# Optimization experiments

Hardware: AMD Instinct MI355X
Metric: run time of the kernel (lower is better)

## Reference

```python
import jax, jax.numpy as jnp
import numpy as np

B, S, D = 8, 1024, 768
H, HD = 12, 64
FF = 3072
EPS = 1e-5


def layernorm(x, w, b):
    mu = jnp.mean(x, axis=-1, keepdims=True)
    var = jnp.mean(jnp.square(x - mu), axis=-1, keepdims=True)
    return (x - mu) / jnp.sqrt(var + EPS) * w + b


def setup_inputs() -> dict:
    key = jax.random.key(0)
    ks = jax.random.split(key, 16)
    s_in = 1.0 / np.sqrt(D)
    s_p = 1.0 / np.sqrt(H * HD)
    s_ff = 1.0 / np.sqrt(FF)
    return {
        "x": jax.random.normal(ks[0], (B, S, D), dtype=jnp.float32),
        "ln1_w": jnp.ones((D,), jnp.float32),
        "ln1_b": jnp.zeros((D,), jnp.float32),
        "Wq": jax.random.uniform(ks[1], (H, D, HD), jnp.float32, -s_in, s_in),
        "bq": jax.random.uniform(ks[2], (H, HD), jnp.float32, -s_in, s_in),
        "Wk": jax.random.uniform(ks[3], (H, D, HD), jnp.float32, -s_in, s_in),
        "bk": jax.random.uniform(ks[4], (H, HD), jnp.float32, -s_in, s_in),
        "Wv": jax.random.uniform(ks[5], (H, D, HD), jnp.float32, -s_in, s_in),
        "bv": jax.random.uniform(ks[6], (H, HD), jnp.float32, -s_in, s_in),
        "Wp": jax.random.uniform(ks[7], (H * HD, D), jnp.float32, -s_p, s_p),
        "bp": jax.random.uniform(ks[8], (D,), jnp.float32, -s_p, s_p),
        "ln2_w": jnp.ones((D,), jnp.float32),
        "ln2_b": jnp.zeros((D,), jnp.float32),
        "W1": jax.random.uniform(ks[9], (D, FF), jnp.float32, -s_in, s_in),
        "b1": jax.random.uniform(ks[10], (FF,), jnp.float32, -s_in, s_in),
        "W2": jax.random.uniform(ks[11], (FF, D), jnp.float32, -s_ff, s_ff),
        "b2": jax.random.uniform(ks[12], (D,), jnp.float32, -s_ff, s_ff),
    }


def reference(x, ln1_w, ln1_b, Wq, bq, Wk, bk, Wv, bv, Wp, bp,
              ln2_w, ln2_b, W1, b1, W2, b2):
    gelu = lambda t: jax.nn.gelu(t, approximate=False)
    # --- multi-head self attention (NOTE: original never applies scale) ---
    y = layernorm(x, ln1_w, ln1_b)                       # [B,S,D]
    q = jnp.einsum('bsd,hde->bhse', y, Wq) + bq[:, None, :][None]
    k = jnp.einsum('bsd,hde->bhse', y, Wk) + bk[:, None, :][None]
    v = jnp.einsum('bsd,hde->bhse', y, Wv) + bv[:, None, :][None]
    attn = jax.nn.softmax(jnp.einsum('bhse,bhte->bhst', q, k), axis=-1)
    out = jnp.einsum('bhst,bhte->bhse', attn, v)         # [B,H,S,HD]
    out = out.transpose(0, 2, 1, 3).reshape(x.shape[0], x.shape[1], -1)  # concat heads
    y = gelu(out @ Wp + bp)                              # projection + GELU
    x = x + y                                            # residual 1
    # --- MLP block ---
    h = layernorm(x, ln2_w, ln2_b)
    h = gelu(h @ W1 + b1)
    h = gelu(h @ W2 + b2)
    return x + h                                         # residual 2
```

## Files before the change

### kernel.cpp

```cpp
#include <hip/hip_runtime.h>
#include <hip/hip_bf16.h>
#include <math.h>

#define BB 8
#define SS 1024
#define DD 768
#define HH 12
#define HDD 64
#define FFF 3072
#define NROW (BB*SS)
#define QKVN (3*DD)

typedef __hip_bfloat16 bf16;
typedef __bf16 bf16x8 __attribute__((ext_vector_type(8)));
typedef float floatx4 __attribute__((ext_vector_type(4)));

__device__ __forceinline__ float gelu_fast(float x) {
    float u = x * fmaf(0.07135481627f, x * x, 1.595769122f);
    float e = __expf(u);
    return x * e * __builtin_amdgcn_rcpf(e + 1.0f);
}

__device__ __forceinline__ unsigned short f2bfbits(float f) {
    bf16 h = __float2bfloat16(f);
    return __builtin_bit_cast(unsigned short, h);
}

__device__ __forceinline__ void gload16(const void* g, void* l) {
    __builtin_amdgcn_global_load_lds(
        (const __attribute__((address_space(1))) unsigned int*)g,
        (__attribute__((address_space(3))) unsigned int*)l, 16, 0, 0);
}

__global__ __launch_bounds__(256) void ln_kernel(const float* __restrict__ x,
                                                 const float* __restrict__ w,
                                                 const float* __restrict__ b,
                                                 bf16* __restrict__ y) {
    int row = blockIdx.x;
    const float* xr = x + (size_t)row * DD;
    bf16* yr = y + (size_t)row * DD;
    int tid = threadIdx.x;
    float v0 = xr[tid], v1 = xr[tid + 256], v2 = xr[tid + 512];
    __shared__ float red[256], red2[256];
    red[tid]  = v0 + v1 + v2;
    red2[tid] = v0*v0 + v1*v1 + v2*v2;
    __syncthreads();
    for (int off = 128; off > 0; off >>= 1) {
        if (tid < off) { red[tid] += red[tid+off]; red2[tid] += red2[tid+off]; }
        __syncthreads();
    }
    float mu  = red[0] * (1.0f / DD);
    float var = red2[0] * (1.0f / DD) - mu * mu;
    float inv = rsqrtf(var + 1e-5f);
    yr[tid]       = __float2bfloat16((v0 - mu) * inv * w[tid]       + b[tid]);
    yr[tid + 256] = __float2bfloat16((v1 - mu) * inv * w[tid + 256] + b[tid + 256]);
    yr[tid + 512] = __float2bfloat16((v2 - mu) * inv * w[tid + 512] + b[tid + 512]);
}

__global__ __launch_bounds__(256) void transpose_cast(
    const float* __restrict__ src, bf16* __restrict__ dst, int K, int N, int hmode)
{
    __shared__ float t[32][33];
    int k0 = blockIdx.x * 32, n0 = blockIdx.y * 32;
    int tx = threadIdx.x & 31, ty4 = threadIdx.x >> 5;
    #pragma unroll
    for (int i = 0; i < 4; i++) {
        int k = k0 + ty4 * 4 + i;
        int n = n0 + tx;
        size_t si = hmode ? ((size_t)(n >> 6) * K * 64 + (size_t)k * 64 + (n & 63))
                          : ((size_t)k * N + n);
        t[ty4 * 4 + i][tx] = src[si];
    }
    __syncthreads();
    #pragma unroll
    for (int i = 0; i < 4; i++) {
        int n = n0 + ty4 * 4 + i;
        int k = k0 + tx;
        dst[(size_t)n * K + k] = __float2bfloat16(t[tx][ty4 * 4 + i]);
    }
}

__global__ void concat_bias(const float* __restrict__ bq, const float* __restrict__ bk,
                            const float* __restrict__ bv, float* __restrict__ dst) {
    int i = blockIdx.x * 256 + threadIdx.x;
    if (i < DD) { dst[i] = bq[i]; dst[DD + i] = bk[i]; dst[2 * DD + i] = bv[i]; }
}

template<int MT, int KH>
__global__ __launch_bounds__(256) void mfma_gemm(
    const bf16* __restrict__ A, const bf16* __restrict__ Bt,
    const float* __restrict__ bias, const float* __restrict__ resid,
    void* __restrict__ Cout, int M, int N, int K, int act, int out_bf16,
    int qkvmode, bf16* __restrict__ qhg, bf16* __restrict__ khg, bf16* __restrict__ vtg)
{
    constexpr int MFRAG = MT / 32;
    constexpr int ACH = MT * 4;
    __shared__ bf16 As[2][KH * MT * 32];
    __shared__ bf16 Bs[2][KH * 128 * 32];
    int tid = threadIdx.x;
    int row0 = blockIdx.y * MT, col0 = blockIdx.x * 128;
    int wave = tid >> 6, lane = tid & 63;
    int wm = (wave >> 1) * (MT / 2), wn = (wave & 1) * 64;
    int l16 = lane & 15, quad = lane >> 4;

    auto stage = [&](int k0, int buf) {
        #pragma unroll
        for (int i = 0; i < ACH * KH / 256; i++) {
            int c = tid + i * 256;
            int half = c / ACH, rem = c % ACH;
            int r = rem >> 2, pos = rem & 3;
            int ksw = k0 + half * 32 + ((pos ^ ((r >> 1) & 3)) << 3);
            gload16(A + (size_t)(row0 + r) * K + ksw, &As[buf][c * 8]);
        }
        #pragma unroll
        for (int i = 0; i < 2 * KH; i++) {
            int c = tid + i * 256;
            int half = c >> 9, rem = c & 511;
            int r = rem >> 2, pos = rem & 3;
            int ksw = k0 + half * 32 + ((pos ^ ((r >> 1) & 3)) << 3);
            gload16(Bt + (size_t)(col0 + r) * K + ksw, &Bs[buf][c * 8]);
        }
    };

    floatx4 acc[MFRAG][4] = {};

    stage(0, 0);
    int cur = 0;
    for (int k0 = 0; k0 < K; k0 += 32 * KH) {
        __syncthreads();
        if (k0 + 32 * KH < K) stage(k0 + 32 * KH, cur ^ 1);
        #pragma unroll
        for (int s = 0; s < KH; s++) {
            bf16x8 af[MFRAG], bfr[4];
            #pragma unroll
            for (int mt = 0; mt < MFRAG; mt++) {
                int r = wm + mt * 16 + l16;
                int pos = quad ^ ((r >> 1) & 3);
                af[mt] = *(const bf16x8*)&As[cur][s * MT * 32 + r * 32 + pos * 8];
            }
            #pragma unroll
            for (int nt = 0; nt < 4; nt++) {
                int r = wn + nt * 16 + l16;
                int pos = quad ^ ((r >> 1) & 3);
                bfr[nt] = *(const bf16x8*)&Bs[cur][s * 4096 + r * 32 + pos * 8];
            }
            #pragma unroll
            for (int mt = 0; mt < MFRAG; mt++)
                #pragma unroll
                for (int nt = 0; nt < 4; nt++)
                    acc[mt][nt] = __builtin_amdgcn_mfma_f32_16x16x32_bf16(
                        af[mt], bfr[nt], acc[mt][nt], 0, 0, 0);
        }
        cur ^= 1;
    }

    if (qkvmode) {
        #pragma unroll
        for (int mt = 0; mt < MFRAG; mt++) {
            int rbase = row0 + wm + mt * 16 + quad * 4;
            int bq_ = rbase >> 10, sb = rbase & 1023;
            #pragma unroll
            for (int nt = 0; nt < 4; nt++) {
                int col = col0 + wn + nt * 16 + l16;
                float bcol = bias[col];
                if (col < DD) {
                    int hh = col >> 6, e = col & 63;
                    bf16* base = qhg + (((size_t)bq_ * HH + hh) * SS + sb) * 64 + e;
                    #pragma unroll
                    for (int r = 0; r < 4; r++)
                        base[(size_t)r * 64] = __float2bfloat16(acc[mt][nt][r] + bcol);
                } else if (col < 2 * DD) {
                    int cc = col - DD, hh = cc >> 6, e = cc & 63;
                    bf16* base = khg + (((size_t)bq_ * HH + hh) * SS) * 64;
                    #pragma unroll
                    for (int r = 0; r < 4; r++) {
                        int s = sb + r;
                        int pos = (((e >> 3) ^ (s & 7)) << 3) | (e & 7);
                        base[(size_t)s * 64 + pos] = __float2bfloat16(acc[mt][nt][r] + bcol);
                    }
                } else {
                    int cc = col - 2 * DD, hh = cc >> 6, e = cc & 63;
                    int c_t = sb >> 3;
                    int sc = (c_t & ~7) | ((c_t & 7) ^ (e & 7));
                    size_t off = (((size_t)bq_ * HH + hh) * 64 + e) * SS + sc * 8 + (sb & 7);
                    ushort4 pk;
                    pk.x = f2bfbits(acc[mt][nt][0] + bcol);
                    pk.y = f2bfbits(acc[mt][nt][1] + bcol);
                    pk.z = f2bfbits(acc[mt][nt][2] + bcol);
                    pk.w = f2bfbits(acc[mt][nt][3] + bcol);
                    *(ushort4*)&vtg[off] = pk;
                }
            }
        }
        return;
    }

    #pragma unroll
    for (int mt = 0; mt < MFRAG; mt++) {
        int rbase = row0 + wm + mt * 16 + quad * 4;
        #pragma unroll
        for (int nt = 0; nt < 4; nt++) {
            int col = col0 + wn + nt * 16 + l16;
            float bcol = bias[col];
            #pragma unroll
            for (int r = 0; r < 4; r++) {
                int row = rbase + r;
                float v = acc[mt][nt][r] + bcol;
                if (act) v = gelu_fast(v);
                if (resid) v += resid[(size_t)row * N + col];
                if (out_bf16) ((bf16*)Cout)[(size_t)row * N + col] = __float2bfloat16(v);
                else          ((float*)Cout)[(size_t)row * N + col] = v;
            }
        }
    }
}

__global__ __launch_bounds__(256) void attn_mfma(
    const bf16* __restrict__ qh, const bf16* __restrict__ kh,
    const bf16* __restrict__ vT, bf16* __restrict__ ao)
{
    __shared__ bf16 Ks[2][64 * 64];
    __shared__ bf16 Vs[2][64 * 64];
    __shared__ bf16 Ps[128 * 64];

    int tid = threadIdx.x;
    int wave = tid >> 6, lane = tid & 63;
    int l16 = lane & 15, quad = lane >> 4;
    int id = blockIdx.x;
    int bh = (id & 7) * 12 + ((id >> 3) >> 3);
    int b = bh / HH, h = bh % HH;
    int s0 = ((id >> 3) & 7) * 128;
    int wm = wave * 32;

    const bf16* qbase = qh + ((size_t)bh * SS) * HDD;
    const bf16* kbase = kh + ((size_t)bh * SS) * HDD;
    const bf16* vbase = vT + ((size_t)bh * HDD) * SS;

    auto stage = [&](int t0, int buf) {
        #pragma unroll
        for (int i = 0; i < 2; i++) {
            int c = tid + i * 256;
            gload16(kbase + (size_t)t0 * 64 + c * 8, &Ks[buf][c * 8]);
            gload16(vbase + (size_t)(c >> 3) * SS + t0 + (c & 7) * 8, &Vs[buf][c * 8]);
        }
    };

    bf16x8 qf[2][2];
    #pragma unroll
    for (int mt = 0; mt < 2; mt++)
        #pragma unroll
        for (int ks = 0; ks < 2; ks++)
            qf[mt][ks] = *(const bf16x8*)(qbase +
                (size_t)(s0 + wm + mt * 16 + l16) * HDD + ks * 32 + quad * 8);

    floatx4 oacc[2][4] = {};
    float lsum[2][4] = {};

    stage(0, 0);
    int cur = 0;
    for (int t0 = 0; t0 < SS; t0 += 64) {
        __syncthreads();
        if (t0 + 64 < SS) stage(t0 + 64, cur ^ 1);

        floatx4 sacc[2][4] = {};
        #pragma unroll
        for (int nt = 0; nt < 4; nt++) {
            int t = nt * 16 + l16;
            #pragma unroll
            for (int ks = 0; ks < 2; ks++) {
                int pos = (quad + 4 * ks) ^ (t & 7);
                bf16x8 bfr = *(const bf16x8*)(&Ks[cur][t * 64 + pos * 8]);
                #pragma unroll
                for (int mt = 0; mt < 2; mt++)
                    sacc[mt][nt] = __builtin_amdgcn_mfma_f32_16x16x32_bf16(
                        qf[mt][ks], bfr, sacc[mt][nt], 0, 0, 0);
            }
        }

        #pragma unroll
        for (int mt = 0; mt < 2; mt++) {
            #pragma unroll
            for (int r = 0; r < 4; r++) {
                float p0 = __expf(sacc[mt][0][r]);
                float p1 = __expf(sacc[mt][1][r]);
                float p2 = __expf(sacc[mt][2][r]);
                float p3 = __expf(sacc[mt][3][r]);
                lsum[mt][r] += (p0 + p1) + (p2 + p3);
                int row = wm + mt * 16 + quad * 4 + r;
                int r7 = row & 7;
                float pv[4] = {p0, p1, p2, p3};
                #pragma unroll
                for (int nt = 0; nt < 4; nt++) {
                    int col = nt * 16 + l16;
                    int pos = (((col >> 3) ^ r7) << 3) | (col & 7);
                    Ps[row * 64 + pos] = __float2bfloat16(pv[nt]);
                }
            }
        }

        #pragma unroll
        for (int mt = 0; mt < 2; mt++) {
            int prow = wm + mt * 16 + l16;
            #pragma unroll
            for (int ks = 0; ks < 2; ks++) {
                int pos = (quad + 4 * ks) ^ (prow & 7);
                bf16x8 pf = *(const bf16x8*)(Ps + prow * 64 + pos * 8);
                #pragma unroll
                for (int nte = 0; nte < 4; nte++) {
                    int e = nte * 16 + l16;
                    int vpos = (quad + 4 * ks) ^ (e & 7);
                    bf16x8 vf = *(const bf16x8*)(&Vs[cur][e * 64 + vpos * 8]);
                    oacc[mt][nte] = __builtin_amdgcn_mfma_f32_16x16x32_bf16(
                        pf, vf, oacc[mt][nte], 0, 0, 0);
                }
            }
        }
        cur ^= 1;
    }

    #pragma unroll
    for (int mt = 0; mt < 2; mt++) {
        #pragma unroll
        for (int r = 0; r < 4; r++) {
            float l = lsum[mt][r];
            #pragma unroll
            for (int d = 1; d < 16; d <<= 1) l += __shfl_xor(l, d, 64);
            float invl = 1.0f / l;
            int srow = s0 + wm + mt * 16 + quad * 4 + r;
            bf16* op = ao + ((size_t)b * SS + srow) * DD + h * HDD;
            #pragma unroll
            for (int nte = 0; nte < 4; nte++)
                op[nte * 16 + l16] = __float2bfloat16(oacc[mt][nte][r] * invl);
        }
    }
}

extern "C" void kernel_launch(void* const* d_in, const int* in_sizes, int n_in,
                              void* d_out, int out_size, void* d_ws, size_t ws_size,
                              hipStream_t stream)
{
    (void)in_sizes; (void)n_in; (void)out_size; (void)ws_size;
    const float* x    = (const float*)d_in[0];
    const float* ln1w = (const float*)d_in[1];
    const float* ln1b = (const float*)d_in[2];
    const float* Wq   = (const float*)d_in[3];
    const float* bq   = (const float*)d_in[4];
    const float* Wk   = (const float*)d_in[5];
    const float* bk   = (const float*)d_in[6];
    const float* Wv   = (const float*)d_in[7];
    const float* bv   = (const float*)d_in[8];
    const float* Wp   = (const float*)d_in[9];
    const float* bp   = (const float*)d_in[10];
    const float* ln2w = (const float*)d_in[11];
    const float* ln2b = (const float*)d_in[12];
    const float* W1   = (const float*)d_in[13];
    const float* b1   = (const float*)d_in[14];
    const float* W2   = (const float*)d_in[15];
    const float* b2   = (const float*)d_in[16];
    float* out = (float*)d_out;

    char* p = (char*)d_ws;
    auto alloc = [&](size_t bytes) { char* r = p; p += (bytes + 255) & ~255ull; return r; };
    bf16*  Wqkvt = (bf16*)alloc((size_t)QKVN * DD * 2);
    bf16*  Wpt   = (bf16*)alloc((size_t)DD * DD * 2);
    bf16*  W1t   = (bf16*)alloc((size_t)FFF * DD * 2);
    bf16*  W2t   = (bf16*)alloc((size_t)DD * FFF * 2);
    float* bqkv  = (float*)alloc((size_t)QKVN * 4);
    bf16*  yb    = (bf16*)alloc((size_t)NROW * DD * 2);
    char*  dynr  = alloc((size_t)NROW * DD * 2 + 3 * ((size_t)NROW * DD * 2));
    bf16*  aob   = (bf16*)dynr;
    bf16*  qhb   = (bf16*)(dynr + (size_t)NROW * DD * 2);
    bf16*  khb   = qhb + (size_t)NROW * DD;
    bf16*  vtb   = khb + (size_t)NROW * DD;
    bf16*  hb    = (bf16*)dynr;

    transpose_cast<<<dim3(DD/32, DD/32),  256, 0, stream>>>(Wq, Wqkvt,            DD, DD, 1);
    transpose_cast<<<dim3(DD/32, DD/32),  256, 0, stream>>>(Wk, Wqkvt + DD*DD,    DD, DD, 1);
    transpose_cast<<<dim3(DD/32, DD/32),  256, 0, stream>>>(Wv, Wqkvt + 2*DD*DD,  DD, DD, 1);
    transpose_cast<<<dim3(DD/32, DD/32),  256, 0, stream>>>(Wp, Wpt,              DD, DD, 0);
    transpose_cast<<<dim3(DD/32, FFF/32), 256, 0, stream>>>(W1, W1t,              DD, FFF, 0);
    transpose_cast<<<dim3(FFF/32, DD/32), 256, 0, stream>>>(W2, W2t,              FFF, DD, 0);
    concat_bias<<<3, 256, 0, stream>>>(bq, bk, bv, bqkv);

    ln_kernel<<<NROW, 256, 0, stream>>>(x, ln1w, ln1b, yb);

    mfma_gemm<128,1><<<dim3(QKVN/128, NROW/128), 256, 0, stream>>>(
        yb, Wqkvt, bqkv, nullptr, nullptr, NROW, QKVN, DD, 0, 0, 1, qhb, khb, vtb);

    attn_mfma<<<dim3(BB*HH*(SS/128)), 256, 0, stream>>>(qhb, khb, vtb, aob);

    mfma_gemm<64,2><<<dim3(DD/128, NROW/64), 256, 0, stream>>>(
        aob, Wpt, bp, x, out, NROW, DD, DD, 1, 0, 0, nullptr, nullptr, nullptr);

    ln_kernel<<<NROW, 256, 0, stream>>>(out, ln2w, ln2b, yb);

    mfma_gemm<128,1><<<dim3(FFF/128, NROW/128), 256, 0, stream>>>(
        yb, W1t, b1, nullptr, hb, NROW, FFF, DD, 1, 1, 0, nullptr, nullptr, nullptr);

    mfma_gemm<64,2><<<dim3(DD/128, NROW/64), 256, 0, stream>>>(
        hb, W2t, b2, out, out, NROW, DD, FFF, 1, 0, 0, nullptr, nullptr, nullptr);
}
```

Baseline: 425.5 us.

## Fuse weight prep kernels, transpose attention MFMA layout, retile FFN1 GEMM

Merges the six weight transpose/cast launches and the bias concat into one prep kernel, cutting launch overhead. Swaps the MFMA operand order in attention (K·Q and V·P) so each lane holds four consecutive columns of one row. That allows packed 64-bit stores of P, a single per-row lsum, and staging the output through LDS for 16-byte coalesced global writes. Also switches the FFN1 GEMM to the 64-row, KH=2 tile configuration.

```diff
diff --git a/kernel.cpp b/kernel.cpp
--- a/kernel.cpp
+++ b/kernel.cpp
@@ -57,11 +57,31 @@
     yr[tid + 512] = __float2bfloat16((v2 - mu) * inv * w[tid + 512] + b[tid + 512]);
 }
 
-__global__ __launch_bounds__(256) void transpose_cast(
-    const float* __restrict__ src, bf16* __restrict__ dst, int K, int N, int hmode)
+__global__ __launch_bounds__(256) void prep_kernel(
+    const float* __restrict__ Wq, const float* __restrict__ Wk,
+    const float* __restrict__ Wv, const float* __restrict__ Wp,
+    const float* __restrict__ W1, const float* __restrict__ W2,
+    const float* __restrict__ bq, const float* __restrict__ bk,
+    const float* __restrict__ bv,
+    bf16* __restrict__ Wqkvt, bf16* __restrict__ Wpt,
+    bf16* __restrict__ W1t, bf16* __restrict__ W2t, float* __restrict__ bqkv)
 {
+    int id = blockIdx.x;
+    if (id >= 6912) {
+        int i = (id - 6912) * 256 + threadIdx.x;
+        if (i < DD) { bqkv[i] = bq[i]; bqkv[DD + i] = bk[i]; bqkv[2*DD + i] = bv[i]; }
+        return;
+    }
+    const float* src; bf16* dst; int K, N, hmode, local;
+    if (id < 1728)      { K = DD;  N = DD;  hmode = 1; local = id % 576;
+                          src = (id < 576) ? Wq : (id < 1152 ? Wk : Wv);
+                          dst = Wqkvt + (size_t)(id / 576) * DD * DD; }
+    else if (id < 2304) { K = DD;  N = DD;  hmode = 0; local = id - 1728; src = Wp; dst = Wpt; }
+    else if (id < 4608) { K = DD;  N = FFF; hmode = 0; local = id - 2304; src = W1; dst = W1t; }
+    else                { K = FFF; N = DD;  hmode = 0; local = id - 4608; src = W2; dst = W2t; }
+    int ktiles = K / 32;
+    int k0 = (local % ktiles) * 32, n0 = (local / ktiles) * 32;
     __shared__ float t[32][33];
-    int k0 = blockIdx.x * 32, n0 = blockIdx.y * 32;
     int tx = threadIdx.x & 31, ty4 = threadIdx.x >> 5;
     #pragma unroll
     for (int i = 0; i < 4; i++) {
@@ -78,12 +98,6 @@
         int k = k0 + tx;
         dst[(size_t)n * K + k] = __float2bfloat16(t[tx][ty4 * 4 + i]);
     }
-}
-
-__global__ void concat_bias(const float* __restrict__ bq, const float* __restrict__ bk,
-                            const float* __restrict__ bv, float* __restrict__ dst) {
-    int i = blockIdx.x * 256 + threadIdx.x;
-    if (i < DD) { dst[i] = bq[i]; dst[DD + i] = bk[i]; dst[2 * DD + i] = bv[i]; }
 }
 
 template<int MT, int KH>
@@ -253,8 +267,8 @@
             qf[mt][ks] = *(const bf16x8*)(qbase +
                 (size_t)(s0 + wm + mt * 16 + l16) * HDD + ks * 32 + quad * 8);
 
-    floatx4 oacc[2][4] = {};
-    float lsum[2][4] = {};
+    floatx4 oaccT[4][2] = {};
+    float lsum[2] = {};
 
     stage(0, 0);
     int cur = 0;
@@ -262,76 +276,88 @@
         __syncthreads();
         if (t0 + 64 < SS) stage(t0 + 64, cur ^ 1);
 
-        floatx4 sacc[2][4] = {};
-        #pragma unroll
-        for (int nt = 0; nt < 4; nt++) {
-            int t = nt * 16 + l16;
+        floatx4 st[4][2] = {};
+        #pragma unroll
+        for (int tt = 0; tt < 4; tt++) {
+            int t = tt * 16 + l16;
             #pragma unroll
             for (int ks = 0; ks < 2; ks++) {
                 int pos = (quad + 4 * ks) ^ (t & 7);
-                bf16x8 bfr = *(const bf16x8*)(&Ks[cur][t * 64 + pos * 8]);
+                bf16x8 kf = *(const bf16x8*)(&Ks[cur][t * 64 + pos * 8]);
                 #pragma unroll
                 for (int mt = 0; mt < 2; mt++)
-                    sacc[mt][nt] = __builtin_amdgcn_mfma_f32_16x16x32_bf16(
-                        qf[mt][ks], bfr, sacc[mt][nt], 0, 0, 0);
-            }
-        }
-
+                    st[tt][mt] = __builtin_amdgcn_mfma_f32_16x16x32_bf16(
+                        kf, qf[mt][ks], st[tt][mt], 0, 0, 0);
+            }
+        }
+
+        #pragma unroll
+        for (int tt = 0; tt < 4; tt++)
+            #pragma unroll
+            for (int mt = 0; mt < 2; mt++) {
+                float p0 = __expf(st[tt][mt][0]);
+                float p1 = __expf(st[tt][mt][1]);
+                float p2 = __expf(st[tt][mt][2]);
+                float p3 = __expf(st[tt][mt][3]);
+                lsum[mt] += (p0 + p1) + (p2 + p3);
+                int m = wm + mt * 16 + l16;
+                int c = tt * 2 + (quad >> 1);
+                ushort4 pk;
+                pk.x = f2bfbits(p0); pk.y = f2bfbits(p1);
+                pk.z = f2bfbits(p2); pk.w = f2bfbits(p3);
+                *(ushort4*)&Ps[m * 64 + ((c ^ (m & 7)) << 3) + (quad & 1) * 4] = pk;
+            }
+
+        #pragma unroll
+        for (int ks = 0; ks < 2; ks++) {
+            bf16x8 pf[2];
+            #pragma unroll
+            for (int mt = 0; mt < 2; mt++) {
+                int m = wm + mt * 16 + l16;
+                pf[mt] = *(const bf16x8*)(&Ps[m * 64 + (((quad + 4 * ks) ^ (m & 7)) << 3)]);
+            }
+            #pragma unroll
+            for (int et = 0; et < 4; et++) {
+                int e = et * 16 + l16;
+                int vpos = (quad + 4 * ks) ^ (e & 7);
+                bf16x8 vf = *(const bf16x8*)(&Vs[cur][e * 64 + vpos * 8]);
+                #pragma unroll
+                for (int mt = 0; mt < 2; mt++)
+                    oaccT[et][mt] = __builtin_amdgcn_mfma_f32_16x16x32_bf16(
+                        vf, pf[mt], oaccT[et][mt], 0, 0, 0);
+            }
+        }
+        cur ^= 1;
+    }
+
+    float linv[2];
+    #pragma unroll
+    for (int mt = 0; mt < 2; mt++) {
+        float l = lsum[mt];
+        l += __shfl_xor(l, 16, 64);
+        l += __shfl_xor(l, 32, 64);
+        linv[mt] = __builtin_amdgcn_rcpf(l);
+    }
+    #pragma unroll
+    for (int et = 0; et < 4; et++)
         #pragma unroll
         for (int mt = 0; mt < 2; mt++) {
-            #pragma unroll
-            for (int r = 0; r < 4; r++) {
-                float p0 = __expf(sacc[mt][0][r]);
-                float p1 = __expf(sacc[mt][1][r]);
-                float p2 = __expf(sacc[mt][2][r]);
-                float p3 = __expf(sacc[mt][3][r]);
-                lsum[mt][r] += (p0 + p1) + (p2 + p3);
-                int row = wm + mt * 16 + quad * 4 + r;
-                int r7 = row & 7;
-                float pv[4] = {p0, p1, p2, p3};
-                #pragma unroll
-                for (int nt = 0; nt < 4; nt++) {
-                    int col = nt * 16 + l16;
-                    int pos = (((col >> 3) ^ r7) << 3) | (col & 7);
-                    Ps[row * 64 + pos] = __float2bfloat16(pv[nt]);
-                }
-            }
-        }
-
-        #pragma unroll
-        for (int mt = 0; mt < 2; mt++) {
-            int prow = wm + mt * 16 + l16;
-            #pragma unroll
-            for (int ks = 0; ks < 2; ks++) {
-                int pos = (quad + 4 * ks) ^ (prow & 7);
-                bf16x8 pf = *(const bf16x8*)(Ps + prow * 64 + pos * 8);
-                #pragma unroll
-                for (int nte = 0; nte < 4; nte++) {
-                    int e = nte * 16 + l16;
-                    int vpos = (quad + 4 * ks) ^ (e & 7);
-                    bf16x8 vf = *(const bf16x8*)(&Vs[cur][e * 64 + vpos * 8]);
-                    oacc[mt][nte] = __builtin_amdgcn_mfma_f32_16x16x32_bf16(
-                        pf, vf, oacc[mt][nte], 0, 0, 0);
-                }
-            }
-        }
-        cur ^= 1;
-    }
-
-    #pragma unroll
-    for (int mt = 0; mt < 2; mt++) {
-        #pragma unroll
-        for (int r = 0; r < 4; r++) {
-            float l = lsum[mt][r];
-            #pragma unroll
-            for (int d = 1; d < 16; d <<= 1) l += __shfl_xor(l, d, 64);
-            float invl = 1.0f / l;
-            int srow = s0 + wm + mt * 16 + quad * 4 + r;
-            bf16* op = ao + ((size_t)b * SS + srow) * DD + h * HDD;
-            #pragma unroll
-            for (int nte = 0; nte < 4; nte++)
-                op[nte * 16 + l16] = __float2bfloat16(oacc[mt][nte][r] * invl);
-        }
+            int m = wm + mt * 16 + l16;
+            int c = et * 2 + (quad >> 1);
+            ushort4 pk;
+            pk.x = f2bfbits(oaccT[et][mt][0] * linv[mt]);
+            pk.y = f2bfbits(oaccT[et][mt][1] * linv[mt]);
+            pk.z = f2bfbits(oaccT[et][mt][2] * linv[mt]);
+            pk.w = f2bfbits(oaccT[et][mt][3] * linv[mt]);
+            *(ushort4*)&Ps[m * 64 + ((c ^ (m & 7)) << 3) + (quad & 1) * 4] = pk;
+        }
+    int mrow = wm + (lane >> 1);
+    bf16* op = ao + ((size_t)b * SS + s0 + mrow) * DD + h * HDD;
+    #pragma unroll
+    for (int i = 0; i < 4; i++) {
+        int j = (lane & 1) * 4 + i;
+        bf16x8 v = *(const bf16x8*)&Ps[mrow * 64 + ((j ^ (mrow & 7)) << 3)];
+        *(bf16x8*)&op[j * 8] = v;
     }
 }
 
@@ -374,13 +400,8 @@
     bf16*  vtb   = khb + (size_t)NROW * DD;
     bf16*  hb    = (bf16*)dynr;
 
-    transpose_cast<<<dim3(DD/32, DD/32),  256, 0, stream>>>(Wq, Wqkvt,            DD, DD, 1);
-    transpose_cast<<<dim3(DD/32, DD/32),  256, 0, stream>>>(Wk, Wqkvt + DD*DD,    DD, DD, 1);
-    transpose_cast<<<dim3(DD/32, DD/32),  256, 0, stream>>>(Wv, Wqkvt + 2*DD*DD,  DD, DD, 1);
-    transpose_cast<<<dim3(DD/32, DD/32),  256, 0, stream>>>(Wp, Wpt,              DD, DD, 0);
-    transpose_cast<<<dim3(DD/32, FFF/32), 256, 0, stream>>>(W1, W1t,              DD, FFF, 0);
-    transpose_cast<<<dim3(FFF/32, DD/32), 256, 0, stream>>>(W2, W2t,              FFF, DD, 0);
-    concat_bias<<<3, 256, 0, stream>>>(bq, bk, bv, bqkv);
+    prep_kernel<<<6915, 256, 0, stream>>>(Wq, Wk, Wv, Wp, W1, W2, bq, bk, bv,
+                                          Wqkvt, Wpt, W1t, W2t, bqkv);
 
     ln_kernel<<<NROW, 256, 0, stream>>>(x, ln1w, ln1b, yb);
 
@@ -394,7 +415,7 @@
 
     ln_kernel<<<NROW, 256, 0, stream>>>(out, ln2w, ln2b, yb);
 
-    mfma_gemm<128,1><<<dim3(FFF/128, NROW/128), 256, 0, stream>>>(
+    mfma_gemm<64,2><<<dim3(FFF/128, NROW/64), 256, 0, stream>>>(
         yb, W1t, b1, nullptr, hb, NROW, FFF, DD, 1, 1, 0, nullptr, nullptr, nullptr);
 
     mfma_gemm<64,2><<<dim3(DD/128, NROW/64), 256, 0, stream>>>(
```

Measured after the change: 396.0 us. -6.9%, faster.
